# Optimization experiments

Measured on AMD Instinct MI355X. Metric: run time of the kernel, lower is better.

Reference implementation:

```python
import jax, jax.numpy as jnp
import numpy as np

CAPACITY_FACTOR = 1.0


def setup_inputs() -> dict:
    key = jax.random.key(0)
    ks = jax.random.split(key, 6)
    B, S, D, H, E = 4, 2048, 1024, 4096, 8
    scale_in = 1.0 / np.sqrt(D)
    scale_h = 1.0 / np.sqrt(H)
    return {
        "inputs": jax.random.normal(ks[0], (B, S, D), dtype=jnp.float32),
        "router_w": jax.random.normal(ks[1], (E, D), dtype=jnp.float32) * scale_in,
        "w1": jax.random.normal(ks[2], (E, D, H), dtype=jnp.float32) * scale_in,
        "b1": jnp.zeros((E, H), dtype=jnp.float32),
        "w2": jax.random.normal(ks[3], (E, H, D), dtype=jnp.float32) * scale_h,
        "b2": jnp.zeros((E, D), dtype=jnp.float32),
    }


def reference(inputs, router_w, w1, b1, w2, b2):
    B, S, D = inputs.shape
    E = router_w.shape[0]
    x = inputs.reshape(-1, D)                     # [T, D], T = B*S
    T = x.shape[0]
    top_k = int(CAPACITY_FACTOR * T / E)          # static: 1024

    # Router + softmax over experts (softmax_topk order), fp32 like the original
    router_logits = x @ router_w.T                # [T, E]
    all_probs = jax.nn.softmax(router_logits.astype(jnp.float32), axis=-1)

    # Expert-choice: each expert picks its top_k tokens
    weights, selected_tokens = jax.lax.top_k(all_probs.T, top_k)  # [E, K]

    # Gather tokens per expert: [E, K, D]
    xg = x[selected_tokens]

    # Per-expert MLP as grouped GEMMs (Linear -> GELU(exact) -> Linear)
    h = jax.nn.gelu(jnp.einsum("ekd,edh->ekh", xg, w1) + b1[:, None, :],
                    approximate=False)
    out = jnp.einsum("ekh,ehd->ekd", h, w2) + b2[:, None, :]   # [E, K, D]

    # Weighted scatter-add combine (indices unique within an expert;
    # cross-expert duplicates accumulate, matching the per-expert += loop)
    out = out * weights[..., None].astype(out.dtype)
    results = jnp.zeros_like(x).at[selected_tokens.reshape(-1)].add(
        out.reshape(-1, D))

    return results.reshape(B, S, D), router_logits, selected_tokens
```

## Files before the change

### kernel.cpp

```cpp
#include <hip/hip_runtime.h>
#include <hip/hip_bf16.h>
#include <math.h>

#define T_TOK 8192
#define E_EXP 8
#define D_DIM 1024
#define H_DIM 4096
#define K_CAP 1024

typedef __attribute__((ext_vector_type(8))) short short8;
typedef __attribute__((ext_vector_type(4))) float floatx4;

typedef __attribute__((address_space(3))) unsigned int lds_u32_t;
typedef __attribute__((address_space(1))) unsigned int gbl_u32_t;
#define ASYNC_CP16(gptr, lptr) \
  __builtin_amdgcn_global_load_lds((gbl_u32_t*)(gptr), (lds_u32_t*)(lptr), 16, 0, 0)

static __device__ __forceinline__ unsigned int f2bf_u(float f) {
  union { float f; unsigned int u; } v; v.f = f;
  unsigned int r = v.u + 0x7FFF + ((v.u >> 16) & 1);
  return r >> 16;
}

__global__ __launch_bounds__(256) void zero_kernel(float* __restrict__ p, int n4) {
  int i = blockIdx.x * 256 + threadIdx.x;
  if (i < n4) ((floatx4*)p)[i] = (floatx4)0.0f;
}

__global__ __launch_bounds__(256)
void convert_kernel(const float* __restrict__ x, unsigned short* __restrict__ xb, int n4) {
  int i = blockIdx.x * 256 + threadIdx.x;
  if (i < n4) {
    float4 v = ((const float4*)x)[i];
    uint2 u;
    u.x = f2bf_u(v.x) | (f2bf_u(v.y) << 16);
    u.y = f2bf_u(v.z) | (f2bf_u(v.w) << 16);
    ((uint2*)xb)[i] = u;
  }
}

template <int KD, int ND>
__global__ __launch_bounds__(256)
void transpose_kernel(const float* __restrict__ w, unsigned short* __restrict__ wt) {
  int e = blockIdx.z;
  int n0 = blockIdx.x * 32, k0 = blockIdx.y * 32;
  __shared__ float ts[32][33];
  int tid = threadIdx.x;
  int r = tid >> 3, c4 = (tid & 7) * 4;
  const float* src = w + ((size_t)e * KD + k0 + r) * ND + n0 + c4;
  float4 v = *(const float4*)src;
  ts[r][c4 + 0] = v.x; ts[r][c4 + 1] = v.y; ts[r][c4 + 2] = v.z; ts[r][c4 + 3] = v.w;
  __syncthreads();
  unsigned int p0 = f2bf_u(ts[c4 + 0][r]) | (f2bf_u(ts[c4 + 1][r]) << 16);
  unsigned int p1 = f2bf_u(ts[c4 + 2][r]) | (f2bf_u(ts[c4 + 3][r]) << 16);
  unsigned short* dst = wt + ((size_t)e * ND + n0 + r) * KD + k0 + c4;
  uint2 u; u.x = p0; u.y = p1;
  *(uint2*)dst = u;
}

__global__ __launch_bounds__(256)
void router_kernel(const float* __restrict__ x, const float* __restrict__ rw,
                   float* __restrict__ logits_out, float* __restrict__ probs_ws,
                   unsigned long long* __restrict__ keys_ws) {
  int t = blockIdx.x;
  int tid = threadIdx.x;
  int lane = tid & 63, wid = tid >> 6;
  __shared__ float xs[D_DIM];
  __shared__ double dred[4 * E_EXP];
  __shared__ double dlog[E_EXP];
  for (int i = tid; i < D_DIM; i += 256) xs[i] = x[(size_t)t * D_DIM + i];
  __syncthreads();
#pragma unroll
  for (int e = 0; e < E_EXP; e++) {
    double s = 0.0;
#pragma unroll
    for (int i = 0; i < 4; i++) {
      int d = tid + i * 256;
      s += (double)xs[d] * (double)rw[e * D_DIM + d];
    }
#pragma unroll
    for (int off = 32; off > 0; off >>= 1) s += __shfl_down(s, off, 64);
    if (lane == 0) dred[wid * E_EXP + e] = s;
  }
  __syncthreads();
  if (tid < E_EXP) {
    double s = dred[tid] + dred[E_EXP + tid] + dred[2 * E_EXP + tid] + dred[3 * E_EXP + tid];
    dlog[tid] = s;
    logits_out[(size_t)t * E_EXP + tid] = (float)s;
  }
  __syncthreads();
  if (tid == 0) {
    double m = dlog[0];
#pragma unroll
    for (int e = 1; e < E_EXP; e++) m = dlog[e] > m ? dlog[e] : m;
    double ex[E_EXP], Z = 0.0;
#pragma unroll
    for (int e = 0; e < E_EXP; e++) { ex[e] = exp(dlog[e] - m); Z += ex[e]; }
#pragma unroll
    for (int e = 0; e < E_EXP; e++) {
      double p = ex[e] / Z;
      probs_ws[e * T_TOK + t] = (float)p;
      unsigned long long b = (unsigned long long)__double_as_longlong(p);
      keys_ws[e * T_TOK + t] = (b & ~8191ULL) | (unsigned long long)(8191 - t);
    }
  }
}

__global__ __launch_bounds__(256)
void topk_kernel(const unsigned long long* __restrict__ keys_ws,
                 const float* __restrict__ probs_ws,
                 int* __restrict__ sel_ws, float* __restrict__ wt_ws,
                 float* __restrict__ selout) {
  int e = blockIdx.x >> 5, seg = blockIdx.x & 31;
  int tid = threadIdx.x;
  const unsigned long long* keys = keys_ws + (size_t)e * T_TOK;
  __shared__ unsigned long long kbuf[2048];
  int t = seg * 256 + tid;
  unsigned long long own = keys[t];
  int rank = 0;
  for (int pass = 0; pass < 4; pass++) {
    __syncthreads();
    for (int j = tid; j < 2048; j += 256) kbuf[j] = keys[pass * 2048 + j];
    __syncthreads();
#pragma unroll 8
    for (int j = 0; j < 2048; j++) rank += (kbuf[j] > own);
  }
  if (rank < K_CAP) {
    sel_ws[e * K_CAP + rank] = t;
    wt_ws[e * K_CAP + rank] = probs_ws[e * T_TOK + t];
    selout[e * K_CAP + rank] = (float)t;
  }
}

template <int MODE, int KDIM, int NDIM>
__global__ __launch_bounds__(256, 2)
void gemm_kernel(const unsigned short* __restrict__ abase,
                 const unsigned short* __restrict__ bt,
                 const float* __restrict__ bias,
                 const int* __restrict__ sel,
                 const float* __restrict__ wt,
                 unsigned short* __restrict__ hout,
                 float* __restrict__ results) {
  int e = blockIdx.z;
  int n0 = blockIdx.x * 128;
  int m0 = blockIdx.y * 128;
  int tid = threadIdx.x;
  int lane = tid & 63, wid = tid >> 6;
  int wave_m = wid >> 1, wave_n = wid & 1;
  __shared__ unsigned short As[128 * 32];
  __shared__ unsigned short Bs[128 * 32];

  int r0 = tid >> 2;
  int coff = (tid & 3) * 8;
  const unsigned short* aptr0;
  const unsigned short* aptr1;
  if (MODE == 1) {
    aptr0 = abase + (size_t)sel[e * K_CAP + m0 + r0] * KDIM + coff;
    aptr1 = abase + (size_t)sel[e * K_CAP + m0 + 64 + r0] * KDIM + coff;
  } else {
    aptr0 = abase + ((size_t)e * K_CAP + m0 + r0) * KDIM + coff;
    aptr1 = aptr0 + (size_t)64 * KDIM;
  }
  const unsigned short* bptr0 = bt + ((size_t)e * NDIM + n0 + r0) * KDIM + coff;
  const unsigned short* bptr1 = bptr0 + (size_t)64 * KDIM;

  char* ldsA0 = (char*)As + wid * 1024;
  char* ldsA1 = ldsA0 + 4096;
  char* ldsB0 = (char*)Bs + wid * 1024;
  char* ldsB1 = ldsB0 + 4096;

  floatx4 acc[4][4];
#pragma unroll
  for (int i = 0; i < 4; i++)
#pragma unroll
    for (int j = 0; j < 4; j++) acc[i][j] = (floatx4)0.0f;

  int lm = lane & 15;
  int q8 = (lane >> 4) * 8;

  for (int k0 = 0; k0 < KDIM; k0 += 32) {
    ASYNC_CP16(aptr0, ldsA0);
    ASYNC_CP16(aptr1, ldsA1);
    ASYNC_CP16(bptr0, ldsB0);
    ASYNC_CP16(bptr1, ldsB1);
    aptr0 += 32; aptr1 += 32; bptr0 += 32; bptr1 += 32;
    __syncthreads();
    short8 av[4], bv[4];
#pragma unroll
    for (int i = 0; i < 4; i++) {
      av[i] = *(const short8*)&As[(wave_m * 64 + i * 16 + lm) * 32 + q8];
      bv[i] = *(const short8*)&Bs[(wave_n * 64 + i * 16 + lm) * 32 + q8];
    }
#pragma unroll
    for (int mi = 0; mi < 4; mi++)
#pragma unroll
      for (int ni = 0; ni < 4; ni++)
        acc[mi][ni] = __builtin_amdgcn_mfma_f32_16x16x32_bf16(av[mi], bv[ni], acc[mi][ni], 0, 0, 0);
    __syncthreads();
  }

  int quad = lane >> 4;
  float bs[4];
#pragma unroll
  for (int ni = 0; ni < 4; ni++)
    bs[ni] = bias[e * NDIM + n0 + wave_n * 64 + ni * 16 + lm];
#pragma unroll
  for (int mi = 0; mi < 4; mi++) {
#pragma unroll
    for (int rg = 0; rg < 4; rg++) {
      int m_l = wave_m * 64 + mi * 16 + quad * 4 + rg;
      int m_g = m0 + m_l;
      if (MODE == 1) {
#pragma unroll
        for (int ni = 0; ni < 4; ni++) {
          int n_l = wave_n * 64 + ni * 16 + lm;
          float v = acc[mi][ni][rg] + bs[ni];
          float gl = 0.5f * v * (1.0f + erff(v * 0.70710678118f));
          hout[((size_t)e * K_CAP + m_g) * H_DIM + n0 + n_l] = (unsigned short)f2bf_u(gl);
        }
      } else {
        int tok = sel[e * K_CAP + m_g];
        float wgt = wt[e * K_CAP + m_g];
#pragma unroll
        for (int ni = 0; ni < 4; ni++) {
          int n_l = wave_n * 64 + ni * 16 + lm;
          float v = (acc[mi][ni][rg] + bs[ni]) * wgt;
          atomicAdd(&results[(size_t)tok * D_DIM + n0 + n_l], v);
        }
      }
    }
  }
}

extern "C" void kernel_launch(void* const* d_in, const int* in_sizes, int n_in,
                              void* d_out, int out_size, void* d_ws, size_t ws_size,
                              hipStream_t stream) {
  const float* x  = (const float*)d_in[0];
  const float* rw = (const float*)d_in[1];
  const float* w1 = (const float*)d_in[2];
  const float* b1 = (const float*)d_in[3];
  const float* w2 = (const float*)d_in[4];
  const float* b2 = (const float*)d_in[5];

  float* out_res = (float*)d_out;
  float* out_log = out_res + (size_t)T_TOK * D_DIM;
  float* out_sel = out_log + (size_t)T_TOK * E_EXP;

  char* ws = (char*)d_ws;
  float* probs_ws = (float*)ws;
  unsigned long long* keys_ws = (unsigned long long*)(ws + 262144);
  int* sel_ws = (int*)(ws + 786432);
  float* wt_ws = (float*)(ws + 819200);
  unsigned short* x_bf = (unsigned short*)(ws + 1048576);
  unsigned short* h_ws = (unsigned short*)(ws + 17825792);
  unsigned short* t_buf = (unsigned short*)(ws + 84934656);

  zero_kernel<<<(T_TOK * D_DIM / 4 + 255) / 256, 256, 0, stream>>>(out_res, T_TOK * D_DIM / 4);

  convert_kernel<<<(T_TOK * D_DIM / 4 + 255) / 256, 256, 0, stream>>>(
      x, x_bf, T_TOK * D_DIM / 4);

  router_kernel<<<T_TOK, 256, 0, stream>>>(x, rw, out_log, probs_ws, keys_ws);

  topk_kernel<<<256, 256, 0, stream>>>(keys_ws, probs_ws, sel_ws, wt_ws, out_sel);

  transpose_kernel<D_DIM, H_DIM><<<dim3(H_DIM / 32, D_DIM / 32, E_EXP), 256, 0, stream>>>(
      w1, t_buf);

  gemm_kernel<1, D_DIM, H_DIM><<<dim3(H_DIM / 128, K_CAP / 128, E_EXP), 256, 0, stream>>>(
      x_bf, t_buf, b1, sel_ws, wt_ws, h_ws, nullptr);

  transpose_kernel<H_DIM, D_DIM><<<dim3(D_DIM / 32, H_DIM / 32, E_EXP), 256, 0, stream>>>(
      w2, t_buf);

  gemm_kernel<2, H_DIM, D_DIM><<<dim3(D_DIM / 128, K_CAP / 128, E_EXP), 256, 0, stream>>>(
      h_ws, t_buf, b2, sel_ws, wt_ws, nullptr, out_res);
}
```

Baseline: 714.9 us.

## Split-K second GEMM, reorder grid expert-major, widen transpose tiles

The second grouped GEMM is split into two K halves accumulated by atomic scatter-add, doubling its block count from 512 to 1024 to fill the GPU better, with bias added only by the first split. Grid indexing is reordered so the expert index is the fastest-varying block dimension, and launch_bounds no longer requests two blocks per CU. The weight transpose kernel now uses 64x64 tiles with 16-byte bf16 stores instead of 32x32 tiles with 8-byte stores. Split-K doubles the atomic traffic into the output and adds rounding-order variation.

```diff
diff --git a/kernel.cpp b/kernel.cpp
--- a/kernel.cpp
+++ b/kernel.cpp
@@ -43,19 +43,30 @@
 __global__ __launch_bounds__(256)
 void transpose_kernel(const float* __restrict__ w, unsigned short* __restrict__ wt) {
   int e = blockIdx.z;
-  int n0 = blockIdx.x * 32, k0 = blockIdx.y * 32;
-  __shared__ float ts[32][33];
-  int tid = threadIdx.x;
-  int r = tid >> 3, c4 = (tid & 7) * 4;
-  const float* src = w + ((size_t)e * KD + k0 + r) * ND + n0 + c4;
-  float4 v = *(const float4*)src;
-  ts[r][c4 + 0] = v.x; ts[r][c4 + 1] = v.y; ts[r][c4 + 2] = v.z; ts[r][c4 + 3] = v.w;
-  __syncthreads();
-  unsigned int p0 = f2bf_u(ts[c4 + 0][r]) | (f2bf_u(ts[c4 + 1][r]) << 16);
-  unsigned int p1 = f2bf_u(ts[c4 + 2][r]) | (f2bf_u(ts[c4 + 3][r]) << 16);
-  unsigned short* dst = wt + ((size_t)e * ND + n0 + r) * KD + k0 + c4;
-  uint2 u; u.x = p0; u.y = p1;
-  *(uint2*)dst = u;
+  int n0 = blockIdx.x * 64, k0 = blockIdx.y * 64;
+  __shared__ float ts[64][65];
+  int tid = threadIdx.x;
+  int rr = tid >> 4;
+  int cc = (tid & 15) * 4;
+  const float* src = w + ((size_t)e * KD + k0 + rr) * ND + n0 + cc;
+#pragma unroll
+  for (int it = 0; it < 4; it++) {
+    float4 v = *(const float4*)(src + (size_t)it * 16 * ND);
+    int r = rr + it * 16;
+    ts[r][cc + 0] = v.x; ts[r][cc + 1] = v.y; ts[r][cc + 2] = v.z; ts[r][cc + 3] = v.w;
+  }
+  __syncthreads();
+  int n = tid >> 3;
+  int k8 = (tid & 7) * 8;
+#pragma unroll
+  for (int it = 0; it < 2; it++) {
+    int nn = n + it * 32;
+    unsigned int u[4];
+#pragma unroll
+    for (int j = 0; j < 4; j++)
+      u[j] = f2bf_u(ts[k8 + 2 * j][nn]) | (f2bf_u(ts[k8 + 2 * j + 1][nn]) << 16);
+    *(uint4*)&wt[((size_t)e * ND + n0 + nn) * KD + k0 + k8] = *(uint4*)u;
+  }
 }
 
 __global__ __launch_bounds__(256)
@@ -132,8 +143,8 @@
   }
 }
 
-template <int MODE, int KDIM, int NDIM>
-__global__ __launch_bounds__(256, 2)
+template <int MODE, int KDIM, int NDIM, int SPLIT, int NT>
+__global__ __launch_bounds__(256)
 void gemm_kernel(const unsigned short* __restrict__ abase,
                  const unsigned short* __restrict__ bt,
                  const float* __restrict__ bias,
@@ -141,9 +152,16 @@
                  const float* __restrict__ wt,
                  unsigned short* __restrict__ hout,
                  float* __restrict__ results) {
-  int e = blockIdx.z;
-  int n0 = blockIdx.x * 128;
-  int m0 = blockIdx.y * 128;
+  int e = blockIdx.x;
+  int rest = blockIdx.y;
+  int s = rest & (SPLIT - 1);
+  int nt = (rest / SPLIT) % NT;
+  int mt = rest / (SPLIT * NT);
+  int n0 = nt * 128;
+  int m0 = mt * 128;
+  const int KCH = KDIM / SPLIT;
+  int kbase = s * KCH;
+
   int tid = threadIdx.x;
   int lane = tid & 63, wid = tid >> 6;
   int wave_m = wid >> 1, wave_n = wid & 1;
@@ -155,13 +173,13 @@
   const unsigned short* aptr0;
   const unsigned short* aptr1;
   if (MODE == 1) {
-    aptr0 = abase + (size_t)sel[e * K_CAP + m0 + r0] * KDIM + coff;
-    aptr1 = abase + (size_t)sel[e * K_CAP + m0 + 64 + r0] * KDIM + coff;
+    aptr0 = abase + (size_t)sel[e * K_CAP + m0 + r0] * KDIM + kbase + coff;
+    aptr1 = abase + (size_t)sel[e * K_CAP + m0 + 64 + r0] * KDIM + kbase + coff;
   } else {
-    aptr0 = abase + ((size_t)e * K_CAP + m0 + r0) * KDIM + coff;
+    aptr0 = abase + ((size_t)e * K_CAP + m0 + r0) * KDIM + kbase + coff;
     aptr1 = aptr0 + (size_t)64 * KDIM;
   }
-  const unsigned short* bptr0 = bt + ((size_t)e * NDIM + n0 + r0) * KDIM + coff;
+  const unsigned short* bptr0 = bt + ((size_t)e * NDIM + n0 + r0) * KDIM + kbase + coff;
   const unsigned short* bptr1 = bptr0 + (size_t)64 * KDIM;
 
   char* ldsA0 = (char*)As + wid * 1024;
@@ -178,7 +196,7 @@
   int lm = lane & 15;
   int q8 = (lane >> 4) * 8;
 
-  for (int k0 = 0; k0 < KDIM; k0 += 32) {
+  for (int k0 = 0; k0 < KCH; k0 += 32) {
     ASYNC_CP16(aptr0, ldsA0);
     ASYNC_CP16(aptr1, ldsA1);
     ASYNC_CP16(bptr0, ldsB0);
@@ -203,7 +221,7 @@
   float bs[4];
 #pragma unroll
   for (int ni = 0; ni < 4; ni++)
-    bs[ni] = bias[e * NDIM + n0 + wave_n * 64 + ni * 16 + lm];
+    bs[ni] = (MODE == 1 || s == 0) ? bias[e * NDIM + n0 + wave_n * 64 + ni * 16 + lm] : 0.0f;
 #pragma unroll
   for (int mi = 0; mi < 4; mi++) {
 #pragma unroll
@@ -264,15 +282,17 @@
 
   topk_kernel<<<256, 256, 0, stream>>>(keys_ws, probs_ws, sel_ws, wt_ws, out_sel);
 
-  transpose_kernel<D_DIM, H_DIM><<<dim3(H_DIM / 32, D_DIM / 32, E_EXP), 256, 0, stream>>>(
+  transpose_kernel<D_DIM, H_DIM><<<dim3(H_DIM / 64, D_DIM / 64, E_EXP), 256, 0, stream>>>(
       w1, t_buf);
 
-  gemm_kernel<1, D_DIM, H_DIM><<<dim3(H_DIM / 128, K_CAP / 128, E_EXP), 256, 0, stream>>>(
+  gemm_kernel<1, D_DIM, H_DIM, 1, H_DIM / 128>
+      <<<dim3(E_EXP, (H_DIM / 128) * (K_CAP / 128)), 256, 0, stream>>>(
       x_bf, t_buf, b1, sel_ws, wt_ws, h_ws, nullptr);
 
-  transpose_kernel<H_DIM, D_DIM><<<dim3(D_DIM / 32, H_DIM / 32, E_EXP), 256, 0, stream>>>(
+  transpose_kernel<H_DIM, D_DIM><<<dim3(D_DIM / 64, H_DIM / 64, E_EXP), 256, 0, stream>>>(
       w2, t_buf);
 
-  gemm_kernel<2, H_DIM, D_DIM><<<dim3(D_DIM / 128, K_CAP / 128, E_EXP), 256, 0, stream>>>(
+  gemm_kernel<2, H_DIM, D_DIM, 2, D_DIM / 128>
+      <<<dim3(E_EXP, (D_DIM / 128) * (K_CAP / 128) * 2), 256, 0, stream>>>(
       h_ws, t_buf, b2, sel_ws, wt_ws, nullptr, out_res);
 }
```

After: 740.5 us. 3.6% more time.
